# Optimization experiments

Measured on AMD Instinct MI355X. Metric: run time of the kernel, lower is better.

Reference implementation:

```python
import jax, jax.numpy as jnp
import numpy as np

B, L, H = 32, 2048, 1024


def setup_inputs() -> dict:
    key = jax.random.key(0)
    ks = jax.random.split(key, 9)
    s = 1.0 / np.sqrt(H)
    return {
        "output": jax.random.normal(ks[0], (B, 1, H), jnp.float32),
        "context": jax.random.normal(ks[1], (B, L, H), jnp.float32),
        "coverage": jax.random.uniform(ks[2], (B, L), jnp.float32),
        # W: Linear(dim, 1)
        "W_w": jax.random.uniform(ks[3], (H,), jnp.float32, -s, s),
        "W_b": jax.random.uniform(ks[4], (), jnp.float32, -s, s),
        # coverage_feature: Linear(1, dim)
        "cov_w": jax.random.uniform(ks[5], (H,), jnp.float32, -1.0, 1.0),
        "cov_b": jax.random.uniform(ks[6], (H,), jnp.float32, -1.0, 1.0),
        # linear_out: Linear(2*dim, dim)
        "out_w": jax.random.uniform(ks[7], (2 * H, H), jnp.float32, -s / np.sqrt(2), s / np.sqrt(2)),
        "out_b": jax.random.uniform(ks[8], (H,), jnp.float32, -s, s),
    }


def reference(output, context, coverage, W_w, W_b, cov_w, cov_b, out_w, out_b):
    # coverage feature: Linear(1, H) applied to coverage[..., None] -> [B, L, H]
    cov_feat = coverage[..., None] * cov_w + cov_b
    # additive score: W(output + context + cov_feat) -> [B, L]
    scores = jnp.einsum('blh,h->bl', output + context + cov_feat, W_w) + W_b
    attn = jax.nn.softmax(scores, axis=1)          # softmax over encoder positions
    coverage_new = coverage + attn                 # [B, L]
    mix = jnp.einsum('bl,blh->bh', attn, context)  # [B, H]
    combined = jnp.concatenate([mix, output[:, 0, :]], axis=-1)  # [B, 2H]
    out = jnp.tanh(combined @ out_w + out_b)[:, None, :]          # [B, 1, H]
    return out, attn[:, None, :], coverage_new
```

## Files before the change

kernel.cpp:

```cpp
#include <hip/hip_runtime.h>
#include <hip/hip_bf16.h>
#include <math.h>

#define BB 32
#define LL 2048
#define HH 1024
#define CPB 32
#define RPW (LL / (CPB * 4))

__device__ __forceinline__ float dot4(float4 a, float4 b) {
    return fmaf(a.x, b.x, fmaf(a.y, b.y, fmaf(a.z, b.z, a.w * b.w)));
}
__device__ __forceinline__ void scal4(float4& a, float s) {
    a.x *= s; a.y *= s; a.z *= s; a.w *= s;
}
__device__ __forceinline__ void fma4(float4& a, float p, float4 x) {
    a.x = fmaf(p, x.x, a.x); a.y = fmaf(p, x.y, a.y);
    a.z = fmaf(p, x.z, a.z); a.w = fmaf(p, x.w, a.w);
}

__global__ __launch_bounds__(256, 4) void k_pass1(
    const float* __restrict__ ctx,
    const float* __restrict__ cov,
    const float* __restrict__ Ww,
    const float* __restrict__ covw,
    float* __restrict__ pbuf,
    float* __restrict__ pz,
    float* __restrict__ pacc)
{
    const int b    = blockIdx.y;
    const int c    = blockIdx.x;
    const int w    = threadIdx.x >> 6;
    const int lane = threadIdx.x & 63;
    const int wib  = c * 4 + w;
    const int l0   = wib * RPW;

    const float4* wwf = (const float4*)Ww;
    float4 w0 = wwf[lane], w1 = wwf[64 + lane], w2 = wwf[128 + lane], w3 = wwf[192 + lane];
    const float4* cwf = (const float4*)covw;
    float c1 = dot4(cwf[lane], w0) + dot4(cwf[64 + lane], w1) +
               dot4(cwf[128 + lane], w2) + dot4(cwf[192 + lane], w3);
#pragma unroll
    for (int s = 32; s; s >>= 1) c1 += __shfl_xor(c1, s);

    float covchunk = (lane < RPW) ? cov[(size_t)b * LL + l0 + lane] : 0.f;

    float Z = 0.f;
    float4 a0 = {0,0,0,0}, a1 = {0,0,0,0}, a2 = {0,0,0,0}, a3 = {0,0,0,0};
    float pkeep = 0.f;
    const float4* rowb = (const float4*)(ctx + ((size_t)b * LL + l0) * HH);

#pragma unroll 2
    for (int r = 0; r < RPW; ++r) {
        const float4* row = rowb + (size_t)r * (HH / 4);
        float4 x0 = row[lane], x1 = row[64 + lane], x2 = row[128 + lane], x3 = row[192 + lane];
        float d = dot4(x0, w0) + dot4(x1, w1) + dot4(x2, w2) + dot4(x3, w3);
#pragma unroll
        for (int s = 32; s; s >>= 1) d += __shfl_xor(d, s);
        float p = __expf(fmaf(c1, __shfl(covchunk, r), d));
        pkeep = (lane == r) ? p : pkeep;
        Z += p;
        fma4(a0, p, x0); fma4(a1, p, x1); fma4(a2, p, x2); fma4(a3, p, x3);
    }

    if (lane < RPW) pbuf[(size_t)b * LL + l0 + lane] = pkeep;

    __shared__ float sacc[4][HH];
    __shared__ float sZ[4];
    float4* ap = (float4*)&sacc[w][0];
    ap[lane] = a0; ap[64 + lane] = a1; ap[128 + lane] = a2; ap[192 + lane] = a3;
    if (lane == 0) sZ[w] = Z;
    __syncthreads();

    const int t = threadIdx.x;
    float4 v0 = ((const float4*)&sacc[0][0])[t];
    float4 v1 = ((const float4*)&sacc[1][0])[t];
    float4 v2 = ((const float4*)&sacc[2][0])[t];
    float4 v3 = ((const float4*)&sacc[3][0])[t];
    float4 v = { v0.x + v1.x + v2.x + v3.x, v0.y + v1.y + v2.y + v3.y,
                 v0.z + v1.z + v2.z + v3.z, v0.w + v1.w + v2.w + v3.w };
    ((float4*)(pacc + ((size_t)b * CPB + c) * HH))[t] = v;
    if (t == 0) pz[b * CPB + c] = sZ[0] + sZ[1] + sZ[2] + sZ[3];
}

__global__ __launch_bounds__(256) void k_combine(
    const float* __restrict__ pz, const float* __restrict__ pacc,
    const float* __restrict__ pbuf, const float* __restrict__ cov,
    float* __restrict__ mix,
    float* __restrict__ out_attn,
    float* __restrict__ out_cov)
{
    const int b = blockIdx.x;
    const int t = threadIdx.x;
    __shared__ float zsh;

    if (t < 64) {
        float z = (t < CPB) ? pz[b * CPB + t] : 0.f;
#pragma unroll
        for (int s = 32; s; s >>= 1) z += __shfl_xor(z, s);
        if (t == 0) zsh = z;
    }
    __syncthreads();
    const float invZ = 1.f / zsh;

    float4 v = {0, 0, 0, 0};
    const float4* pb = (const float4*)(pacc + (size_t)b * CPB * HH);
#pragma unroll 4
    for (int i = 0; i < CPB; ++i) {
        float4 a = pb[(size_t)i * (HH / 4) + t];
        v.x += a.x; v.y += a.y; v.z += a.z; v.w += a.w;
    }
    scal4(v, invZ);
    ((float4*)(mix + (size_t)b * HH))[t] = v;

    for (int l = t; l < LL; l += 256) {
        float a = pbuf[(size_t)b * LL + l] * invZ;
        out_attn[(size_t)b * LL + l] = a;
        out_cov[(size_t)b * LL + l] = cov[(size_t)b * LL + l] + a;
    }
}

__global__ __launch_bounds__(256) void k_gemm_part(
    const float* __restrict__ mix,
    const float* __restrict__ outp,
    const float* __restrict__ W,
    float* __restrict__ part)
{
    const int h0 = blockIdx.x * 128;
    const int kc = blockIdx.y;
    const int k0 = kc * 64;
    __shared__ float comb[64][40];

    const int t = threadIdx.x;
    {
        const int kk = t & 63;
        const int bb = t >> 6;
        const float* src = (k0 < HH) ? (mix + k0) : (outp + (k0 - HH));
        for (int b2 = bb; b2 < BB; b2 += 4)
            comb[kk][b2] = src[(size_t)b2 * HH + kk];
    }
    __syncthreads();

    const int hg = t & 31;
    const int bg = t >> 5;
    const float* Wp = W + (size_t)k0 * HH + h0 + hg * 4;

    float4 acc0 = {0,0,0,0}, acc1 = {0,0,0,0}, acc2 = {0,0,0,0}, acc3 = {0,0,0,0};
#pragma unroll 4
    for (int kk = 0; kk < 64; ++kk) {
        float4 c = *(const float4*)&comb[kk][bg * 4];
        float4 w = *(const float4*)(Wp + (size_t)kk * HH);
        fma4(acc0, c.x, w); fma4(acc1, c.y, w);
        fma4(acc2, c.z, w); fma4(acc3, c.w, w);
    }

    float* pp = part + ((size_t)kc * BB + bg * 4) * HH + h0 + hg * 4;
    *(float4*)(pp + 0 * HH) = acc0;
    *(float4*)(pp + 1 * HH) = acc1;
    *(float4*)(pp + 2 * HH) = acc2;
    *(float4*)(pp + 3 * HH) = acc3;
}

__global__ __launch_bounds__(256) void k_final(
    const float* __restrict__ part,
    const float* __restrict__ outb,
    float* __restrict__ out0)
{
    const int idx4 = blockIdx.x * 256 + threadIdx.x;
    const int b  = idx4 >> 8;
    const int h4 = idx4 & 255;
    float4 s = {0, 0, 0, 0};
#pragma unroll 8
    for (int kc = 0; kc < 32; ++kc) {
        float4 p = ((const float4*)part)[((size_t)kc * BB + b) * 256 + h4];
        s.x += p.x; s.y += p.y; s.z += p.z; s.w += p.w;
    }
    float4 bb = ((const float4*)outb)[h4];
    float4 o;
    o.x = tanhf(s.x + bb.x); o.y = tanhf(s.y + bb.y);
    o.z = tanhf(s.z + bb.z); o.w = tanhf(s.w + bb.w);
    ((float4*)out0)[idx4] = o;
}

extern "C" void kernel_launch(void* const* d_in, const int* in_sizes, int n_in,
                              void* d_out, int out_size, void* d_ws, size_t ws_size,
                              hipStream_t stream) {
    const float* outp = (const float*)d_in[0];
    const float* ctx  = (const float*)d_in[1];
    const float* cov  = (const float*)d_in[2];
    const float* Ww   = (const float*)d_in[3];
    const float* covw = (const float*)d_in[5];
    const float* outw = (const float*)d_in[7];
    const float* outb = (const float*)d_in[8];

    float* out0     = (float*)d_out;
    float* out_attn = out0 + BB * HH;
    float* out_cov  = out_attn + BB * LL;

    float* w = (float*)d_ws;
    float* pbuf = w;  w += (size_t)BB * LL;
    float* pz   = w;  w += (size_t)BB * CPB;
    float* pacc = w;  w += (size_t)BB * CPB * HH;
    float* mix  = w;  w += (size_t)BB * HH;
    float* part = w;

    dim3 g1(CPB, BB);
    k_pass1<<<g1, 256, 0, stream>>>(ctx, cov, Ww, covw, pbuf, pz, pacc);
    k_combine<<<BB, 256, 0, stream>>>(pz, pacc, pbuf, cov, mix, out_attn, out_cov);
    dim3 g3(8, 32);
    k_gemm_part<<<g3, 256, 0, stream>>>(mix, outp, outw, part);
    k_final<<<32, 256, 0, stream>>>(part, outb, out0);
}
```

Measured before the change: 75.50 us.

## Use 512-thread pass1 blocks with nontemporal loads and parallelize combine/final

The main pass now uses 8 waves per block with 8 rows each, keeping the 32 chunks per batch, and streams context rows with nontemporal loads so they do not pollute the cache. The combine kernel is split across 6 blocks per batch: four reduce column slices of the partial accumulators and two write the attention and coverage outputs. The final kernel splits the 32-way reduction across lane pairs and combines them with a shuffle, doubling the block count. The aim is more parallelism and memory-level parallelism in the small tail kernels, at the cost of larger blocks and more shared memory per block in pass1.

```diff
diff --git a/kernel.cpp b/kernel.cpp
--- a/kernel.cpp
+++ b/kernel.cpp
@@ -5,8 +5,11 @@
 #define BB 32
 #define LL 2048
 #define HH 1024
-#define CPB 32
-#define RPW (LL / (CPB * 4))
+#define WPB 8
+#define RPW 8
+#define CPB (LL / (WPB * RPW))
+
+typedef float fx4 __attribute__((ext_vector_type(4)));
 
 __device__ __forceinline__ float dot4(float4 a, float4 b) {
     return fmaf(a.x, b.x, fmaf(a.y, b.y, fmaf(a.z, b.z, a.w * b.w)));
@@ -18,8 +21,15 @@
     a.x = fmaf(p, x.x, a.x); a.y = fmaf(p, x.y, a.y);
     a.z = fmaf(p, x.z, a.z); a.w = fmaf(p, x.w, a.w);
 }
-
-__global__ __launch_bounds__(256, 4) void k_pass1(
+__device__ __forceinline__ void add4(float4& a, float4 x) {
+    a.x += x.x; a.y += x.y; a.z += x.z; a.w += x.w;
+}
+__device__ __forceinline__ float4 ntload4(const float4* p) {
+    fx4 v = __builtin_nontemporal_load((const fx4*)p);
+    return make_float4(v.x, v.y, v.z, v.w);
+}
+
+__global__ __launch_bounds__(512, 6) void k_pass1(
     const float* __restrict__ ctx,
     const float* __restrict__ cov,
     const float* __restrict__ Ww,
@@ -32,8 +42,7 @@
     const int c    = blockIdx.x;
     const int w    = threadIdx.x >> 6;
     const int lane = threadIdx.x & 63;
-    const int wib  = c * 4 + w;
-    const int l0   = wib * RPW;
+    const int l0   = c * (WPB * RPW) + w * RPW;
 
     const float4* wwf = (const float4*)Ww;
     float4 w0 = wwf[lane], w1 = wwf[64 + lane], w2 = wwf[128 + lane], w3 = wwf[192 + lane];
@@ -53,7 +62,10 @@
 #pragma unroll 2
     for (int r = 0; r < RPW; ++r) {
         const float4* row = rowb + (size_t)r * (HH / 4);
-        float4 x0 = row[lane], x1 = row[64 + lane], x2 = row[128 + lane], x3 = row[192 + lane];
+        float4 x0 = ntload4(row + lane);
+        float4 x1 = ntload4(row + 64 + lane);
+        float4 x2 = ntload4(row + 128 + lane);
+        float4 x3 = ntload4(row + 192 + lane);
         float d = dot4(x0, w0) + dot4(x1, w1) + dot4(x2, w2) + dot4(x3, w3);
 #pragma unroll
         for (int s = 32; s; s >>= 1) d += __shfl_xor(d, s);
@@ -65,22 +77,26 @@
 
     if (lane < RPW) pbuf[(size_t)b * LL + l0 + lane] = pkeep;
 
-    __shared__ float sacc[4][HH];
-    __shared__ float sZ[4];
+    __shared__ float sacc[WPB][HH];
+    __shared__ float sZ[WPB];
     float4* ap = (float4*)&sacc[w][0];
     ap[lane] = a0; ap[64 + lane] = a1; ap[128 + lane] = a2; ap[192 + lane] = a3;
     if (lane == 0) sZ[w] = Z;
     __syncthreads();
 
     const int t = threadIdx.x;
-    float4 v0 = ((const float4*)&sacc[0][0])[t];
-    float4 v1 = ((const float4*)&sacc[1][0])[t];
-    float4 v2 = ((const float4*)&sacc[2][0])[t];
-    float4 v3 = ((const float4*)&sacc[3][0])[t];
-    float4 v = { v0.x + v1.x + v2.x + v3.x, v0.y + v1.y + v2.y + v3.y,
-                 v0.z + v1.z + v2.z + v3.z, v0.w + v1.w + v2.w + v3.w };
-    ((float4*)(pacc + ((size_t)b * CPB + c) * HH))[t] = v;
-    if (t == 0) pz[b * CPB + c] = sZ[0] + sZ[1] + sZ[2] + sZ[3];
+    if (t < 256) {
+        float4 v = {0, 0, 0, 0};
+#pragma unroll
+        for (int i = 0; i < WPB; ++i) add4(v, ((const float4*)&sacc[i][0])[t]);
+        ((float4*)(pacc + ((size_t)b * CPB + c) * HH))[t] = v;
+    }
+    if (t == 0) {
+        float z = 0.f;
+#pragma unroll
+        for (int i = 0; i < WPB; ++i) z += sZ[i];
+        pz[b * CPB + c] = z;
+    }
 }
 
 __global__ __launch_bounds__(256) void k_combine(
@@ -91,8 +107,10 @@
     float* __restrict__ out_cov)
 {
     const int b = blockIdx.x;
+    const int y = blockIdx.y;
     const int t = threadIdx.x;
     __shared__ float zsh;
+    __shared__ float4 red[4][64];
 
     if (t < 64) {
         float z = (t < CPB) ? pz[b * CPB + t] : 0.f;
@@ -103,20 +121,30 @@
     __syncthreads();
     const float invZ = 1.f / zsh;
 
-    float4 v = {0, 0, 0, 0};
-    const float4* pb = (const float4*)(pacc + (size_t)b * CPB * HH);
-#pragma unroll 4
-    for (int i = 0; i < CPB; ++i) {
-        float4 a = pb[(size_t)i * (HH / 4) + t];
-        v.x += a.x; v.y += a.y; v.z += a.z; v.w += a.w;
-    }
-    scal4(v, invZ);
-    ((float4*)(mix + (size_t)b * HH))[t] = v;
-
-    for (int l = t; l < LL; l += 256) {
-        float a = pbuf[(size_t)b * LL + l] * invZ;
-        out_attn[(size_t)b * LL + l] = a;
-        out_cov[(size_t)b * LL + l] = cov[(size_t)b * LL + l] + a;
+    if (y < 4) {
+        const int col = y * 64 + (t & 63);
+        const int g = t >> 6;
+        const float4* pb = (const float4*)(pacc + (size_t)b * CPB * HH);
+        float4 v = {0, 0, 0, 0};
+#pragma unroll
+        for (int i = g * 8; i < g * 8 + 8; ++i)
+            add4(v, pb[(size_t)i * (HH / 4) + col]);
+        red[g][t & 63] = v;
+        __syncthreads();
+        if (t < 64) {
+            float4 s = red[0][t];
+            add4(s, red[1][t]); add4(s, red[2][t]); add4(s, red[3][t]);
+            scal4(s, invZ);
+            ((float4*)(mix + (size_t)b * HH))[y * 64 + t] = s;
+        }
+    } else {
+        const int base = (y - 4) * (LL / 2);
+        for (int l = t; l < LL / 2; l += 256) {
+            const size_t idx = (size_t)b * LL + base + l;
+            float a = pbuf[idx] * invZ;
+            out_attn[idx] = a;
+            out_cov[idx] = cov[idx] + a;
+        }
     }
 }
 
@@ -166,20 +194,26 @@
     const float* __restrict__ outb,
     float* __restrict__ out0)
 {
-    const int idx4 = blockIdx.x * 256 + threadIdx.x;
-    const int b  = idx4 >> 8;
-    const int h4 = idx4 & 255;
+    const int g = blockIdx.x * 256 + threadIdx.x;
+    const int o = g >> 1;
+    const int half = g & 1;
+    const int b  = o >> 8;
+    const int h4 = o & 255;
     float4 s = {0, 0, 0, 0};
-#pragma unroll 8
-    for (int kc = 0; kc < 32; ++kc) {
-        float4 p = ((const float4*)part)[((size_t)kc * BB + b) * 256 + h4];
-        s.x += p.x; s.y += p.y; s.z += p.z; s.w += p.w;
-    }
-    float4 bb = ((const float4*)outb)[h4];
-    float4 o;
-    o.x = tanhf(s.x + bb.x); o.y = tanhf(s.y + bb.y);
-    o.z = tanhf(s.z + bb.z); o.w = tanhf(s.w + bb.w);
-    ((float4*)out0)[idx4] = o;
+#pragma unroll
+    for (int kc = half * 16; kc < half * 16 + 16; ++kc)
+        add4(s, ((const float4*)part)[((size_t)kc * BB + b) * 256 + h4]);
+    s.x += __shfl_xor(s.x, 1);
+    s.y += __shfl_xor(s.y, 1);
+    s.z += __shfl_xor(s.z, 1);
+    s.w += __shfl_xor(s.w, 1);
+    if (half == 0) {
+        float4 bb = ((const float4*)outb)[h4];
+        float4 out;
+        out.x = tanhf(s.x + bb.x); out.y = tanhf(s.y + bb.y);
+        out.z = tanhf(s.z + bb.z); out.w = tanhf(s.w + bb.w);
+        ((float4*)out0)[o] = out;
+    }
 }
 
 extern "C" void kernel_launch(void* const* d_in, const int* in_sizes, int n_in,
@@ -205,9 +239,10 @@
     float* part = w;
 
     dim3 g1(CPB, BB);
-    k_pass1<<<g1, 256, 0, stream>>>(ctx, cov, Ww, covw, pbuf, pz, pacc);
-    k_combine<<<BB, 256, 0, stream>>>(pz, pacc, pbuf, cov, mix, out_attn, out_cov);
+    k_pass1<<<g1, 512, 0, stream>>>(ctx, cov, Ww, covw, pbuf, pz, pacc);
+    dim3 g2(BB, 6);
+    k_combine<<<g2, 256, 0, stream>>>(pz, pacc, pbuf, cov, mix, out_attn, out_cov);
     dim3 g3(8, 32);
     k_gemm_part<<<g3, 256, 0, stream>>>(mix, outp, outw, part);
-    k_final<<<32, 256, 0, stream>>>(part, outb, out0);
-}
+    k_final<<<64, 256, 0, stream>>>(part, outb, out0);
+}
```

Measured after the change: 79.28 us. 1.05x slower.
